# Kernel tuning notes

Hardware: AMD Instinct MI355X
Metric: run time of the kernel (lower is better)

## Reference

```python
import jax, jax.numpy as jnp
import numpy as np

SCALES = [1.0, 0.9, 1.1]


def conv2d(x, w, stride=1, pad=0):
    return jax.lax.conv_general_dilated(
        x, w, (stride, stride), [(pad, pad), (pad, pad)],
        dimension_numbers=('NCHW', 'OIHW', 'NCHW'))


def resize_hp(x, h, w):
    """Half-pixel bilinear == F.interpolate(mode='bilinear', align_corners=False)."""
    return jax.image.resize(x, x.shape[:-2] + (h, w), method='bilinear', antialias=False)


def upsample2x_ac(x):
    """align_corners=True bilinear 2x == nn.UpsamplingBilinear2d(scale_factor=2)."""
    def interp(arr, axis):
        n_in = arr.shape[axis]
        n_out = 2 * n_in
        pos = jnp.linspace(0.0, n_in - 1.0, n_out)
        i0 = jnp.floor(pos).astype(jnp.int32)
        i1 = jnp.minimum(i0 + 1, n_in - 1)
        t = (pos - i0.astype(pos.dtype)).astype(arr.dtype)
        shp = [1] * arr.ndim
        shp[axis] = n_out
        t = t.reshape(shp)
        return jnp.take(arr, i0, axis=axis) * (1 - t) + jnp.take(arr, i1, axis=axis) * t
    return interp(interp(x, 2), 3)


def backbone(images, fw1, fw2, fw3, fw4):
    # Stand-in for Resnet50FPN: two maps at stride 8 (512ch) and stride 16 (1024ch).
    x = jax.nn.relu(conv2d(images, fw1, 2, 3))   # stride 2
    x = jax.nn.relu(conv2d(x, fw2, 2, 1))        # stride 4
    f3 = jax.nn.relu(conv2d(x, fw3, 2, 1))       # stride 8,  C=512
    f4 = jax.nn.relu(conv2d(f3, fw4, 2, 1))      # stride 16, C=1024
    return [f3, f4]


def extract_features(image_features, tlbrs_np, H):
    # Faithful port of extract_features: per-batch/per-map/per-patch crop ->
    # bilinear resize -> multi-scale conv2d correlation. Crop coords come from
    # the concrete tlbrs array (data-dependent shapes, resolved at trace time).
    B, P, _ = tlbrs_np.shape
    batch_similarities = []
    for b in range(B):
        similarities = []
        for feat in image_features:
            fm = feat[b:b + 1]                                  # [1,FC,FH,FW]
            _, FC, FH, FW = fm.shape
            scaling = H / FH
            sc = tlbrs_np[b] / scaling
            tl = np.maximum(np.floor(sc[:, :2]), 0.0)
            br = np.ceil(sc[:, 2:]) + 1.0
            br[:, 0] = np.minimum(br[:, 0], FH)
            br[:, 1] = np.minimum(br[:, 1], FW)
            PH = int((br[:, 0] - tl[:, 0]).max())
            PW = int((br[:, 1] - tl[:, 1]).max())
            patches = []
            for p in range(P):
                top, left = int(tl[p, 0]), int(tl[p, 1])
                bot, right = int(br[p, 0]), int(br[p, 1])
                patches.append(resize_hp(fm[:, :, top:bot, left:right], PH, PW))
            patches = jnp.concatenate(patches, axis=0)          # [P,FC,PH,PW]
            for scale in SCALES:
                PHs = int(np.ceil(PH * scale))
                PWs = int(np.ceil(PW * scale))
                if PHs < 1:
                    PHs = PH
                if PWs < 1:
                    PWs = PW
                pf = resize_hp(patches, PHs, PWs)
                # F.pad(left=PWs//2, right=(PWs-1)//2, top=PHs//2, bottom=(PHs-1)//2)
                sim = jax.lax.conv_general_dilated(
                    fm, pf, (1, 1),
                    [(PHs // 2, (PHs - 1) // 2), (PWs // 2, (PWs - 1) // 2)],
                    dimension_numbers=('NCHW', 'OIHW', 'NCHW'))  # [1,P,FH,FW]
                sim = jnp.transpose(sim, (1, 0, 2, 3))           # [P,1,FH,FW]
                similarities.append(resize_hp(sim, FH, FW))
        SH = max(s_.shape[2] for s_ in similarities)
        SW = max(s_.shape[3] for s_ in similarities)
        sims = jnp.concatenate([resize_hp(s_, SH, SW) for s_ in similarities], axis=1)
        batch_similarities.append(sims)                          # [P,S,SH,SW]
    return jnp.stack(batch_similarities, axis=0)                 # [B,P,S,SH,SW]


def count_regressor(x, rw1, rb1, rw2, rb2, rw3, rb3, rw4, rb4, rw5, rb5):
    bc = lambda v: v[None, :, None, None]
    x = jax.nn.relu(conv2d(x, rw1, 1, 3) + bc(rb1))   # 6  -> 196, k7 p3
    x = upsample2x_ac(x)
    x = jax.nn.relu(conv2d(x, rw2, 1, 2) + bc(rb2))   # 196 -> 128, k5 p2
    x = upsample2x_ac(x)
    x = jax.nn.relu(conv2d(x, rw3, 1, 1) + bc(rb3))   # 128 -> 64, k3 p1
    x = upsample2x_ac(x)
    x = jax.nn.relu(conv2d(x, rw4, 1, 0) + bc(rb4))   # 64  -> 32, k1
    x = jax.nn.relu(conv2d(x, rw5, 1, 0) + bc(rb5))   # 32  -> 1,  k1
    return x


def setup_inputs() -> dict:
    key = jax.random.key(0)
    ks = jax.random.split(key, 10)
    B, P, H, W = 2, 3, 384, 384

    def w(k, shape):
        fan_in = shape[1] * shape[2] * shape[3]
        return (jax.random.normal(k, shape, jnp.float32)
                * np.float32(np.sqrt(2.0 / fan_in)))

    images = jax.random.normal(ks[0], (B, 3, H, W), jnp.float32)
    rng = np.random.RandomState(0)
    t = rng.uniform(20, 260, (B, P))
    l = rng.uniform(20, 260, (B, P))
    bh = rng.uniform(32, 96, (B, P))
    bw = rng.uniform(32, 96, (B, P))
    tlbrs = jnp.asarray(
        np.stack([t, l, np.minimum(t + bh, H), np.minimum(l + bw, W)], axis=-1),
        jnp.float32)
    return dict(
        images=images, tlbrs=tlbrs,
        fw1=w(ks[1], (64, 3, 7, 7)), fw2=w(ks[2], (256, 64, 3, 3)),
        fw3=w(ks[3], (512, 256, 3, 3)), fw4=w(ks[4], (1024, 512, 3, 3)),
        rw1=w(ks[5], (196, 6, 7, 7)), rb1=jnp.zeros((196,), jnp.float32),
        rw2=w(ks[6], (128, 196, 5, 5)), rb2=jnp.zeros((128,), jnp.float32),
        rw3=w(ks[7], (64, 128, 3, 3)), rb3=jnp.zeros((64,), jnp.float32),
        rw4=w(ks[8], (32, 64, 1, 1)), rb4=jnp.zeros((32,), jnp.float32),
        rw5=w(ks[9], (1, 32, 1, 1)), rb5=jnp.zeros((1,), jnp.float32))


def reference(images, tlbrs, fw1, fw2, fw3, fw4,
              rw1, rb1, rw2, rb2, rw3, rb3, rw4, rb4, rw5, rb5):
    H = images.shape[2]
    feats = backbone(images, fw1, fw2, fw3, fw4)
    sims = extract_features(feats, np.asarray(tlbrs), H)        # [B,P,S,SH,SW]
    B, P, S, SH, SW = sims.shape
    x = sims.reshape(B * P, S, SH, SW)
    out = count_regressor(x, rw1, rb1, rw2, rb2, rw3, rb3, rw4, rb4, rw5, rb5)
    oh, ow = out.shape[2], out.shape[3]
    # pool='max' over the P exemplar maps, per batch element
    return out.reshape(B, P, 1, oh, ow).max(axis=1)             # [B,1,8*SH,8*SW]
```

## Files before the change

### kernel.cpp

```cpp
#include <hip/hip_runtime.h>
#include <math.h>

typedef _Float16 h8 __attribute__((ext_vector_type(8)));
typedef float f4 __attribute__((ext_vector_type(4)));

static const size_t OFF_SIMSH = 256;
static const size_t OFF_WB    = 98560;
static const size_t ARENA     = 3553536;
static const size_t IMH  = 3553536;
static const size_t B1H  = 4833536;
static const size_t B2H  = 7602432;
static const size_t F3H  = 10813696;
static const size_t F4H  = 13467904;
static const size_t PRAW = 15827200;
static const size_t PSC  = 18186496;
static const size_t SIMRAW = 27144448;
static const size_t WSIM = 27196288;
static const size_t R1H = 3553536;
static const size_t U1H = 6011136;
static const size_t R2H = 13537536;
static const size_t U2H = 17076480;
static const size_t R3H = 33683712;

static const size_t WB1 = 0;
static const size_t WB2 = 28672;
static const size_t WB3 = 176128;
static const size_t WB4 = 1355776;
static const size_t WR1 = 6074368;
static const size_t WR2 = 6189056;
static const size_t WR3 = 6836224;

__global__ __launch_bounds__(64) void k_meta(const float* __restrict__ tlbrs,
                                             int* __restrict__ meta)
{
    if (threadIdx.x != 0 || blockIdx.x != 0) return;
    const double SC[3] = {1.0, 0.9, 1.1};
    for (int b = 0; b < 2; ++b)
        for (int lvl = 0; lvl < 2; ++lvl) {
            int FH = lvl ? 24 : 48;
            float scaling = lvl ? 16.f : 8.f;
            int base = (b * 2 + lvl) * 32;
            int PH = 0, PW = 0;
            for (int p = 0; p < 3; ++p) {
                const float* t4 = tlbrs + (b * 3 + p) * 4;
                float st = t4[0] / scaling, sl = t4[1] / scaling;
                float sb = t4[2] / scaling, sr = t4[3] / scaling;
                int top  = (int)fmaxf(floorf(st), 0.f);
                int left = (int)fmaxf(floorf(sl), 0.f);
                int bot  = (int)fminf(ceilf(sb) + 1.f, (float)FH);
                int rgt  = (int)fminf(ceilf(sr) + 1.f, (float)FH);
                meta[base + p * 4 + 0] = top;
                meta[base + p * 4 + 1] = left;
                meta[base + p * 4 + 2] = bot;
                meta[base + p * 4 + 3] = rgt;
                PH = max(PH, bot - top);
                PW = max(PW, rgt - left);
            }
            meta[base + 12] = PH;
            meta[base + 13] = PW;
            for (int s = 0; s < 3; ++s) {
                int PHs = (int)ceil((double)PH * SC[s]);
                int PWs = (int)ceil((double)PW * SC[s]);
                if (PHs < 1) PHs = PH;
                if (PWs < 1) PWs = PW;
                meta[base + 14 + s * 2] = PHs;
                meta[base + 15 + s * 2] = PWs;
            }
        }
}

__device__ __forceinline__ void halo_zero(h8* base, int Hp, int Wp, int halo,
                                          int Cg, int N)
{
    int inner = Hp - 2 * halo;
    int frame = Hp * Wp - inner * inner;
    long total = (long)N * frame * Cg;
    long idx = (long)blockIdx.x * 256 + threadIdx.x;
    if (idx >= total) return;
    int cg = (int)(idx % Cg);
    long r = idx / Cg;
    int f = (int)(r % frame);
    int n = (int)(r / frame);
    int topN = halo * Wp;
    int y, x;
    if (f < topN) { y = f / Wp; x = f % Wp; }
    else if (f < 2 * topN) { int f2 = f - topN; y = Hp - halo + f2 / Wp; x = f2 % Wp; }
    else {
        int f3 = f - 2 * topN;
        int row = f3 / (2 * halo), rr = f3 - row * (2 * halo);
        y = halo + row;
        x = rr < halo ? rr : Wp - 2 * halo + rr;
    }
    h8 z;
#pragma unroll
    for (int j = 0; j < 8; ++j) z[j] = (_Float16)0.f;
    base[((long)n * Hp * Wp + (long)y * Wp + x) * Cg + cg] = z;
}

__global__ __launch_bounds__(256) void k_halos1(float* wsf)
{
    switch (blockIdx.y) {
    case 0: halo_zero((h8*)(wsf + IMH), 400, 400, 8, 1, 2); break;
    case 1: halo_zero((h8*)(wsf + B1H), 208, 208, 8, 8, 2); break;
    case 2: halo_zero((h8*)(wsf + B2H), 112, 112, 8, 32, 2); break;
    case 3: halo_zero((h8*)(wsf + F3H), 72, 72, 12, 64, 2); break;
    default: halo_zero((h8*)(wsf + F4H), 48, 48, 12, 128, 2); break;
    }
}

__global__ __launch_bounds__(256) void k_halos2(float* wsf)
{
    switch (blockIdx.y) {
    case 0: halo_zero((h8*)(wsf + OFF_SIMSH), 64, 64, 8, 1, 6); break;
    case 1: halo_zero((h8*)(wsf + R1H), 64, 64, 8, 25, 6); break;
    case 2: halo_zero((h8*)(wsf + U1H), 112, 112, 8, 25, 6); break;
    default: halo_zero((h8*)(wsf + U2H), 208, 208, 8, 16, 6); break;
    }
}

__global__ __launch_bounds__(256) void k_im2hwc(const float* __restrict__ img,
    _Float16* __restrict__ o)
{
    int idx = blockIdx.x * 256 + threadIdx.x;
    if (idx >= 2359296) return;
    int c = idx & 7;
    int pix = (idx >> 3) % 147456;
    int b = (idx >> 3) / 147456;
    int y = pix / 384, x = pix - y * 384;
    float v = (c < 3) ? img[((size_t)b * 3 + c) * 147456 + pix] : 0.f;
    o[((size_t)b * 1280000 + ((size_t)(y + 8) * 400 + (x + 8)) * 8) + c] = (_Float16)v;
}

__global__ __launch_bounds__(256) void k_wprepH(const float* __restrict__ w,
    _Float16* __restrict__ wB, int Cin, int KKt, int Cinp, int Cout, int Coutp,
    int total)
{
    int idx = blockIdx.x * 256 + threadIdx.x;
    if (idx >= total) return;
    int j = idx & 7;
    int co = (idx >> 3) % Coutp;
    int kq = idx / (8 * Coutp);
    int k = kq * 8 + j;
    int tap = k / Cinp, cip = k - tap * Cinp;
    float v = 0.f;
    if (tap < KKt && cip < Cin && co < Cout)
        v = w[((size_t)co * Cin + cip) * KKt + tap];
    wB[idx] = (_Float16)v;
}

template<int KK, int KW, int S, int CINP, int MT>
__global__ __launch_bounds__(256, 3) void k_convH(
    const _Float16* __restrict__ inI, int Winp, long inStride,
    const _Float16* __restrict__ wB, const float* __restrict__ bias,
    _Float16* __restrict__ outI, int Wop, long outStride,
    int Cout, int Coutp, int Wout, int pad, int Kpad, int storeC,
    float dsc, float osc)
{
    const int tid = threadIdx.x;
    const int n_img = blockIdx.z;
    const int m0 = blockIdx.x * (MT * 64);
    const int co0 = blockIdx.y * 64;
    const _Float16* inb = inI + (size_t)n_img * inStride;

    const int wv = tid >> 6, lane = tid & 63;
    const int lq = lane >> 4, lr = lane & 15;

    const _Float16* pb[MT];
#pragma unroll
    for (int mt = 0; mt < MT; ++mt) {
        int m = m0 + (wv * MT + mt) * 16 + lr;
        int y = m / Wout, x = m - y * Wout;
        pb[mt] = inb + ((long)(y * S - pad) * Winp + (x * S - pad)) * CINP;
    }
    const _Float16* wbc = wB + (size_t)(co0 + lr) * 8;

    f4 acc[MT][4];
#pragma unroll
    for (int i = 0; i < MT; ++i)
#pragma unroll
        for (int j = 0; j < 4; ++j) { f4 z = {0.f, 0.f, 0.f, 0.f}; acc[i][j] = z; }

    const int Kbat = Kpad >> 6;

    auto load_step = [&](int kb, h8* afX, h8* bfX) {
        int k0 = kb * 32 + lq * 8;
        int tap = k0 / CINP;
        int ci0 = k0 - tap * CINP;
        int dy = tap / KW, dx = tap - dy * KW;
        size_t kq = (size_t)(kb * 4 + lq) * Coutp;
#pragma unroll
        for (int nt = 0; nt < 4; ++nt)
            bfX[nt] = *(const h8*)(wbc + (kq + nt * 16) * 8);
        int doff = (dy * Winp + dx) * CINP + ci0;
#pragma unroll
        for (int mt = 0; mt < MT; ++mt)
            afX[mt] = *(const h8*)(pb[mt] + doff);
    };
    auto mfma_step = [&](h8* afX, h8* bfX) {
#pragma unroll
        for (int mt = 0; mt < MT; ++mt)
#pragma unroll
            for (int nt = 0; nt < 4; ++nt)
                acc[mt][nt] = __builtin_amdgcn_mfma_f32_16x16x32_f16(
                    afX[mt], bfX[nt], acc[mt][nt], 0, 0, 0);
    };
    auto load_batch = [&](int bb, h8 afX[2][MT > 0 ? MT : 1], h8 bfX[2][4]) {
        load_step(2 * bb, afX[0], bfX[0]);
        load_step(2 * bb + 1, afX[1], bfX[1]);
    };
    auto mfma_batch = [&](h8 afX[2][MT > 0 ? MT : 1], h8 bfX[2][4]) {
        mfma_step(afX[0], bfX[0]);
        mfma_step(afX[1], bfX[1]);
    };

    h8 afA[2][MT > 0 ? MT : 1], bfA[2][4], afB[2][MT > 0 ? MT : 1], bfB[2][4];
    load_batch(0, afA, bfA);
    int bb = 0;
    for (; bb + 1 < Kbat; bb += 2) {
        load_batch(bb + 1, afB, bfB);
        mfma_batch(afA, bfA);
        if (bb + 2 < Kbat) load_batch(bb + 2, afA, bfA);
        mfma_batch(afB, bfB);
    }
    if (bb < Kbat) mfma_batch(afA, bfA);

    _Float16* ob = outI + (size_t)n_img * outStride;
#pragma unroll
    for (int nt = 0; nt < 4; ++nt) {
        int co = co0 + nt * 16 + lr;
        if (co >= storeC) continue;
        bool valid = co < Cout;
        float bv = (bias && valid) ? bias[co] : 0.f;
#pragma unroll
        for (int mt = 0; mt < MT; ++mt) {
#pragma unroll
            for (int reg = 0; reg < 4; ++reg) {
                int m = m0 + (wv * MT + mt) * 16 + lq * 4 + reg;
                int y = m / Wout, x = m - y * Wout;
                float v = valid
                    ? fmaxf(fmaf(acc[mt][nt][reg], dsc, bv), 0.f) * osc : 0.f;
                ob[((long)y * Wop + x) * storeC + co] = (_Float16)v;
            }
        }
    }
}

__global__ __launch_bounds__(256) void k_praw(const _Float16* __restrict__ f3hI,
    const _Float16* __restrict__ f4hI, const int* __restrict__ meta,
    float* __restrict__ praw)
{
    int z = blockIdx.z;
    int p = z % 3, m = z / 3, lvl = m % 2, b = m / 2;
    int c = blockIdx.y;
    int FC = lvl ? 1024 : 512;
    if (c >= FC) return;
    int FHp = lvl ? 48 : 72;
    int fsh = lvl ? 10 : 9;
    const int* mb = meta + m * 32;
    int PH = mb[12], PW = mb[13];
    int oy = threadIdx.x / 16, ox = threadIdx.x % 16;
    if (oy >= PH || ox >= PW) return;
    int top = mb[p * 4 + 0], left = mb[p * 4 + 1];
    int bot = mb[p * 4 + 2], rgt = mb[p * 4 + 3];
    int h = bot - top, w = rgt - left;
    const _Float16* fm = lvl ? (f4hI + (size_t)b * 2359296)
                             : (f3hI + (size_t)b * 2654208);
    float sy = ((oy + 0.5f) * h) / PH - 0.5f;
    sy = fminf(fmaxf(sy, 0.f), (float)(h - 1));
    int y0 = (int)floorf(sy); float ty = sy - y0; int y1 = min(y0 + 1, h - 1);
    float sx = ((ox + 0.5f) * w) / PW - 0.5f;
    sx = fminf(fmaxf(sx, 0.f), (float)(w - 1));
    int x0 = (int)floorf(sx); float tx = sx - x0; int x1 = min(x0 + 1, w - 1);
    float v00 = (float)fm[((size_t)((top + y0) * FHp + (left + x0)) << fsh) + c];
    float v01 = (float)fm[((size_t)((top + y0) * FHp + (left + x1)) << fsh) + c];
    float v10 = (float)fm[((size_t)((top + y1) * FHp + (left + x0)) << fsh) + c];
    float v11 = (float)fm[((size_t)((top + y1) * FHp + (left + x1)) << fsh) + c];
    float v = (1.f - ty) * ((1.f - tx) * v00 + tx * v01)
            +        ty  * ((1.f - tx) * v10 + tx * v11);
    size_t base = (size_t)(b * 1179648 + (lvl ? 393216 : 0)) + ((size_t)p * FC + c) * 256;
    praw[base + oy * 16 + ox] = v;
}

__global__ __launch_bounds__(256) void k_psc(const float* __restrict__ praw,
    const int* __restrict__ meta, float* __restrict__ psc)
{
    int z = blockIdx.z;
    int p = z % 3, s = (z / 3) % 3, lvl = (z / 9) % 2, b = z / 18;
    int c = blockIdx.y;
    int FC = lvl ? 1024 : 512;
    if (c >= FC) return;
    const int* mb = meta + (b * 2 + lvl) * 32;
    int PH = mb[12], PW = mb[13];
    int PHs = mb[14 + s * 2], PWs = mb[15 + s * 2];
    int idx = blockIdx.x * 256 + threadIdx.x;
    int ys = idx / 18, xs = idx % 18;
    if (ys >= PHs || xs >= PWs) return;
    const float* src = praw + (size_t)(b * 1179648 + (lvl ? 393216 : 0))
                            + ((size_t)p * FC + c) * 256;
    float sy = ((ys + 0.5f) * PH) / PHs - 0.5f;
    sy = fminf(fmaxf(sy, 0.f), (float)(PH - 1));
    int y0 = (int)floorf(sy); float ty = sy - y0; int y1 = min(y0 + 1, PH - 1);
    float sx = ((xs + 0.5f) * PW) / PWs - 0.5f;
    sx = fminf(fmaxf(sx, 0.f), (float)(PW - 1));
    int x0 = (int)floorf(sx); float tx = sx - x0; int x1 = min(x0 + 1, PW - 1);
    float v = (1.f - ty) * ((1.f - tx) * src[y0 * 16 + x0] + tx * src[y0 * 16 + x1])
            +        ty  * ((1.f - tx) * src[y1 * 16 + x0] + tx * src[y1 * 16 + x1]);
    size_t base = (size_t)b * 4478976 + (lvl ? (1492992 + (size_t)s * 995328)
                                             : ((size_t)s * 497664));
    psc[base + ((size_t)p * FC + c) * 324 + ys * 18 + xs] = v;
}

__global__ __launch_bounds__(256) void k_fill0(float* p, int n)
{
    int i = blockIdx.x * 256 + threadIdx.x;
    if (i < n) p[i] = 0.f;
}

__global__ __launch_bounds__(256) void k_wsim(const float* __restrict__ psc,
    const int* __restrict__ meta, _Float16* __restrict__ W)
{
    int z = blockIdx.z;
    int lvl = z & 1, b = z >> 1;
    int FC = lvl ? 1024 : 512;
    int total = FC * 324 * 16;
    int e = blockIdx.x * 256 + threadIdx.x;
    if (e >= total) return;
    _Float16* Wz = W + (size_t)b * 7962624 + (lvl ? 2654208 : 0);
    int j = e & 7, n = (e >> 3) & 15, kq = e >> 7;
    int k = kq * 8 + j;
    int ci = k & 15;
    int tapcb = k >> 4;
    int tap = tapcb % 324;
    int cb = tapcb / 324;
    int c = cb * 16 + ci;
    int rr = tap / 18, cc = tap - rr * 18;
    float v = 0.f;
    if (n < 9) {
        int s = n / 3, p = n % 3;
        const int* mb = meta + z * 32;
        int PHs = mb[14 + s * 2], PWs = mb[15 + s * 2];
        int ky = rr - (9 - (PHs >> 1));
        int kx = cc - (9 - (PWs >> 1));
        if ((unsigned)ky < (unsigned)PHs && (unsigned)kx < (unsigned)PWs) {
            size_t base = (size_t)b * 4478976 + (lvl ? (1492992 + (size_t)s * 995328)
                                                     : ((size_t)s * 497664));
            v = psc[base + ((size_t)p * FC + c) * 324 + ky * 18 + kx];
        }
    }
    Wz[e] = (_Float16)v;
}

template<int TW, int FH, int FHP, int FC, int SROWS, int SCOLSU, bool LVL>
__global__ __launch_bounds__(256) void k_simS(
    const _Float16* __restrict__ fI, long fStride,
    const _Float16* __restrict__ Wb, float* __restrict__ simraw)
{
    __shared__ __align__(16) _Float16 As[2 * SROWS * SCOLSU * 8];
    const int M = FH * FH;
    const int PIX = TW * 64;
    const int b = blockIdx.z;
    const int mg = blockIdx.x;
    const int cb = blockIdx.y;
    const _Float16* fm = fI + (size_t)b * fStride;
    const _Float16* Wz = Wb + (size_t)b * 7962624 + (LVL ? 2654208 : 0)
                       + (size_t)cb * 82944;
    const int tid = threadIdx.x;
    const int y0row = (mg * PIX) / FH;

    const int count = 2 * SROWS * SCOLSU;
    for (int idx = tid; idx < count; idx += 256) {
        int half = idx / (SROWS * SCOLSU);
        int rem = idx - half * (SROWS * SCOLSU);
        int row = rem / SCOLSU, col = rem - row * SCOLSU;
        const _Float16* src = fm + ((long)(y0row + row - 9) * FHP + (col - 9)) * FC
                            + cb * 16 + half * 8;
        *(h8*)&As[idx * 8] = *(const h8*)src;
    }
    __syncthreads();

    const int wv = tid >> 6, lane = tid & 63;
    const int lq = lane >> 4, lr = lane & 15;
    int abase[TW];
#pragma unroll
    for (int i = 0; i < TW; ++i) {
        int st = mg * (4 * TW) + wv + 4 * i;
        int m = st * 16 + lr;
        int py = m / FH - y0row, px = m - (m / FH) * FH;
        abase[i] = ((lq & 1) * SROWS + py) * SCOLSU + px;
    }
    const int thalf = lq >> 1;

    f4 acc[TW];
#pragma unroll
    for (int i = 0; i < TW; ++i) { f4 z = {0.f, 0.f, 0.f, 0.f}; acc[i] = z; }

    auto load_step = [&](int step, h8* avX, h8& bfX) {
        int tap = step * 2 + thalf;
        int dy = tap / 18, dx = tap - dy * 18;
        bfX = *(const h8*)(Wz + ((size_t)(step * 4 + lq) * 16 + lr) * 8);
        int doff = dy * SCOLSU + dx;
#pragma unroll
        for (int i = 0; i < TW; ++i)
            avX[i] = *(const h8*)&As[(size_t)(abase[i] + doff) * 8];
    };
    auto mfma_step = [&](h8* avX, h8 bfX) {
#pragma unroll
        for (int i = 0; i < TW; ++i)
            acc[i] = __builtin_amdgcn_mfma_f32_16x16x32_f16(avX[i], bfX, acc[i], 0, 0, 0);
    };

    h8 avA[TW], avB[TW], bfA, bfB;
    load_step(0, avA, bfA);
    int kb = 0;
    for (; kb + 1 < 162; kb += 2) {
        load_step(kb + 1, avB, bfB);
        mfma_step(avA, bfA);
        if (kb + 2 < 162) load_step(kb + 2, avA, bfA);
        mfma_step(avB, bfB);
    }
    if (kb < 162) mfma_step(avA, bfA);

    if (lr < 9) {
        int s = lr / 3, p = lr - s * 3;
        float* base = simraw + (size_t)b * 25920
                    + (LVL ? (20736 + (size_t)s * 1728) : ((size_t)s * 6912))
                    + (size_t)p * M;
#pragma unroll
        for (int i = 0; i < TW; ++i) {
            int st = mg * (4 * TW) + wv + 4 * i;
            int row0 = st * 16 + lq * 4;
#pragma unroll
            for (int r = 0; r < 4; ++r) {
                int m = row0 + r;
                if (m < M) atomicAdd(base + m, acc[i][r]);
            }
        }
    }
}

__global__ __launch_bounds__(256) void k_sims(const float* __restrict__ simraw,
    _Float16* __restrict__ simshI)
{
    int idx = blockIdx.x * 256 + threadIdx.x;
    if (idx >= 110592) return;
    int scat = idx & 7;
    int rest = idx >> 3;
    int x = rest % 48, y = (rest / 48) % 48;
    int p = (rest / 2304) % 3, b = rest / 6912;
    float v = 0.f;
    if (scat < 6) {
        int lvl = scat / 3, s = scat % 3;
        if (lvl == 0) {
            v = simraw[(size_t)b * 25920 + (size_t)s * 6912 + (size_t)p * 2304 + y * 48 + x];
        } else {
            const float* src = simraw + (size_t)b * 25920 + 20736 + (size_t)s * 1728
                                      + (size_t)p * 576;
            float sy = (y + 0.5f) * 0.5f - 0.5f; sy = fminf(fmaxf(sy, 0.f), 23.f);
            int y0 = (int)floorf(sy); float ty = sy - y0; int y1 = min(y0 + 1, 23);
            float sx = (x + 0.5f) * 0.5f - 0.5f; sx = fminf(fmaxf(sx, 0.f), 23.f);
            int x0 = (int)floorf(sx); float tx = sx - x0; int x1 = min(x0 + 1, 23);
            v = (1.f - ty) * ((1.f - tx) * src[y0 * 24 + x0] + tx * src[y0 * 24 + x1])
              +        ty  * ((1.f - tx) * src[y1 * 24 + x0] + tx * src[y1 * 24 + x1]);
        }
    }
    int n = b * 3 + p;
    simshI[((size_t)n * 32768 + ((size_t)y * 64 + x) * 8) + scat]
        = (_Float16)(v * 0.0009765625f);
}

__global__ __launch_bounds__(256) void k_up2acH(const h8* __restrict__ inI,
    int inWp, long inStride, h8* __restrict__ outI, int outWp, long outStride,
    int N_, int Hin, int Win, int Cg)
{
    int Hout = 2 * Hin, Wout = 2 * Win;
    size_t total = (size_t)N_ * Hout * Wout * Cg;
    size_t idx = (size_t)blockIdx.x * 256 + threadIdx.x;
    if (idx >= total) return;
    int cg = (int)(idx % Cg);
    size_t r = idx / Cg;
    int x = (int)(r % Wout);
    int y = (int)((r / Wout) % Hout);
    int n = (int)(r / ((size_t)Wout * Hout));
    int dh = 2 * Hin - 1, dw = 2 * Win - 1;
    int ay = y * (Hin - 1);
    int y0 = ay / dh; int y1 = min(y0 + 1, Hin - 1);
    float ty = (float)(ay - y0 * dh) / (float)dh;
    int ax = x * (Win - 1);
    int x0 = ax / dw; int x1 = min(x0 + 1, Win - 1);
    float tx = (float)(ax - x0 * dw) / (float)dw;
    const h8* base = inI + (size_t)n * inStride;
    h8 a = base[((size_t)y0 * inWp + x0) * Cg + cg];
    h8 b8 = base[((size_t)y0 * inWp + x1) * Cg + cg];
    h8 c8 = base[((size_t)y1 * inWp + x0) * Cg + cg];
    h8 d8 = base[((size_t)y1 * inWp + x1) * Cg + cg];
    float w00 = (1.f - ty) * (1.f - tx), w01 = (1.f - ty) * tx;
    float w10 = ty * (1.f - tx), w11 = ty * tx;
    h8 o;
#pragma unroll
    for (int j = 0; j < 8; ++j)
        o[j] = (_Float16)(w00 * (float)a[j] + w01 * (float)b8[j]
                        + w10 * (float)c8[j] + w11 * (float)d8[j]);
    outI[(size_t)n * outStride + ((size_t)y * outWp + x) * Cg + cg] = o;
}

__global__ __launch_bounds__(256) void k_final(const h8* __restrict__ r3h,
    const float* __restrict__ w4, const float* __restrict__ b4,
    const float* __restrict__ w5, const float* __restrict__ b5,
    float* __restrict__ out)
{
    __shared__ float sw4[2048];
    __shared__ float sb4[32];
    __shared__ float sw5[32];
    int tid = threadIdx.x;
    for (int i = tid; i < 2048; i += 256) sw4[i] = w4[i];
    if (tid < 32) { sb4[tid] = b4[tid]; sw5[tid] = w5[tid]; }
    __syncthreads();
    int idx = blockIdx.x * 256 + tid;
    int x = idx % 384, y = (idx / 384) % 384, b = idx / 147456;
    int ay = y * 191; int y0 = ay / 383; int y1 = min(y0 + 1, 191);
    float ty = (float)(ay - y0 * 383) / 383.f;
    int ax = x * 191; int x0 = ax / 383; int x1 = min(x0 + 1, 191);
    float tx = (float)(ax - x0 * 383) / 383.f;
    float w00 = (1.f - ty) * (1.f - tx), w01 = (1.f - ty) * tx;
    float w10 = ty * (1.f - tx), w11 = ty * tx;
    float best = 0.f;
    for (int p = 0; p < 3; ++p) {
        int n = b * 3 + p;
        float acc[32];
#pragma unroll
        for (int co = 0; co < 32; ++co) acc[co] = sb4[co];
        const h8* rb = r3h + (size_t)n * 36864 * 8;
        for (int cg = 0; cg < 8; ++cg) {
            h8 a00 = rb[(size_t)(y0 * 192 + x0) * 8 + cg];
            h8 a01 = rb[(size_t)(y0 * 192 + x1) * 8 + cg];
            h8 a10 = rb[(size_t)(y1 * 192 + x0) * 8 + cg];
            h8 a11 = rb[(size_t)(y1 * 192 + x1) * 8 + cg];
#pragma unroll
            for (int jj = 0; jj < 8; ++jj) {
                float v = (w00 * (float)a00[jj] + w01 * (float)a01[jj]
                         + w10 * (float)a10[jj] + w11 * (float)a11[jj]) * 64.f;
                int ci = cg * 8 + jj;
#pragma unroll
                for (int co = 0; co < 32; ++co)
                    acc[co] = fmaf(sw4[co * 64 + ci], v, acc[co]);
            }
        }
        float s5 = b5[0];
#pragma unroll
        for (int co = 0; co < 32; ++co)
            s5 = fmaf(fmaxf(acc[co], 0.f), sw5[co], s5);
        s5 = fmaxf(s5, 0.f);
        best = fmaxf(best, s5);
    }
    out[idx] = best;
}

extern "C" void kernel_launch(void* const* d_in, const int* in_sizes, int n_in,
                              void* d_out, int out_size, void* d_ws, size_t ws_size,
                              hipStream_t stream)
{
    (void)in_sizes; (void)n_in; (void)out_size; (void)ws_size;
    const float* images = (const float*)d_in[0];
    const float* tlbrs  = (const float*)d_in[1];
    const float* fw1 = (const float*)d_in[2];
    const float* fw2 = (const float*)d_in[3];
    const float* fw3 = (const float*)d_in[4];
    const float* fw4 = (const float*)d_in[5];
    const float* rw1 = (const float*)d_in[6];
    const float* rb1 = (const float*)d_in[7];
    const float* rw2 = (const float*)d_in[8];
    const float* rb2 = (const float*)d_in[9];
    const float* rw3 = (const float*)d_in[10];
    const float* rb3 = (const float*)d_in[11];
    const float* rw4 = (const float*)d_in[12];
    const float* rb4 = (const float*)d_in[13];
    const float* rw5 = (const float*)d_in[14];
    const float* rb5 = (const float*)d_in[15];
    float* wsf = (float*)d_ws;
    int* meta = (int*)d_ws;
    float* out = (float*)d_out;
    _Float16* wb = (_Float16*)(wsf + OFF_WB);

    _Float16* imhI   = (_Float16*)(wsf + IMH)  + (8 * 400 + 8) * 8;
    _Float16* b1hI   = (_Float16*)(wsf + B1H)  + (8 * 208 + 8) * 64;
    _Float16* b2hI   = (_Float16*)(wsf + B2H)  + (8 * 112 + 8) * 256;
    _Float16* f3hI   = (_Float16*)(wsf + F3H)  + (12 * 72 + 12) * 512;
    _Float16* f4hI   = (_Float16*)(wsf + F4H)  + (12 * 48 + 12) * 1024;
    _Float16* simshI = (_Float16*)(wsf + OFF_SIMSH) + (8 * 64 + 8) * 8;
    _Float16* r1hI   = (_Float16*)(wsf + R1H)  + (8 * 64 + 8) * 200;
    _Float16* u1hI   = (_Float16*)(wsf + U1H)  + (8 * 112 + 8) * 200;
    _Float16* r2h    = (_Float16*)(wsf + R2H);
    _Float16* u2hI   = (_Float16*)(wsf + U2H)  + (8 * 208 + 8) * 128;
    _Float16* r3h    = (_Float16*)(wsf + R3H);
    _Float16* wsim   = (_Float16*)(wsf + WSIM);

    const float INV64 = 1.f / 64.f;

    hipLaunchKernelGGL(k_halos1, dim3(1728, 5), dim3(256), 0, stream, wsf);
    hipLaunchKernelGGL(k_meta, dim3(1), dim3(64), 0, stream, tlbrs, meta);
    hipLaunchKernelGGL(k_im2hwc, dim3(9216), dim3(256), 0, stream, images,
        (_Float16*)(wsf + IMH));

    hipLaunchKernelGGL(k_wprepH, dim3(112), dim3(256), 0, stream,
        fw1, wb + WB1, 3, 49, 8, 64, 64, 28672);
    hipLaunchKernelGGL(k_wprepH, dim3(576), dim3(256), 0, stream,
        fw2, wb + WB2, 64, 9, 64, 256, 256, 147456);
    hipLaunchKernelGGL(k_wprepH, dim3(4608), dim3(256), 0, stream,
        fw3, wb + WB3, 256, 9, 256, 512, 512, 1179648);
    hipLaunchKernelGGL(k_wprepH, dim3(18432), dim3(256), 0, stream,
        fw4, wb + WB4, 512, 9, 512, 1024, 1024, 4718592);
    hipLaunchKernelGGL(k_wprepH, dim3(448), dim3(256), 0, stream,
        rw1, wb + WR1, 6, 49, 8, 196, 256, 114688);
    hipLaunchKernelGGL(k_wprepH, dim3(2528), dim3(256), 0, stream,
        rw2, wb + WR2, 196, 25, 200, 128, 128, 647168);
    hipLaunchKernelGGL(k_wprepH, dim3(288), dim3(256), 0, stream,
        rw3, wb + WR3, 128, 9, 128, 64, 64, 73728);

    hipLaunchKernelGGL((k_convH<49, 7, 2, 8, 2>), dim3(288, 1, 2), dim3(256), 0, stream,
        imhI, 400, 1280000L, wb + WB1, (const float*)nullptr,
        b1hI, 208, 2768896L, 64, 64, 192, 3, 448, 64, 1.f, 1.f);
    hipLaunchKernelGGL((k_convH<9, 3, 2, 64, 2>), dim3(72, 4, 2), dim3(256), 0, stream,
        b1hI, 208, 2768896L, wb + WB2, (const float*)nullptr,
        b2hI, 112, 3211264L, 256, 256, 96, 1, 576, 256, 1.f, 1.f);
    hipLaunchKernelGGL((k_convH<9, 3, 2, 256, 2>), dim3(18, 8, 2), dim3(256), 0, stream,
        b2hI, 112, 3211264L, wb + WB3, (const float*)nullptr,
        f3hI, 72, 2654208L, 512, 512, 48, 1, 2304, 512, 1.f, 1.f);
    hipLaunchKernelGGL((k_convH<9, 3, 2, 512, 1>), dim3(9, 16, 2), dim3(256), 0, stream,
        f3hI, 72, 2654208L, wb + WB4, (const float*)nullptr,
        f4hI, 48, 2359296L, 1024, 1024, 24, 1, 4608, 1024, 1.f, 1.f);

    hipLaunchKernelGGL(k_praw, dim3(1, 1024, 12), dim3(256), 0, stream,
        f3hI, f4hI, meta, wsf + PRAW);
    hipLaunchKernelGGL(k_psc, dim3(2, 1024, 36), dim3(256), 0, stream,
        wsf + PRAW, meta, wsf + PSC);
    hipLaunchKernelGGL(k_wsim, dim3(20736, 1, 4), dim3(256), 0, stream,
        wsf + PSC, meta, wsim);
    hipLaunchKernelGGL(k_fill0, dim3(203), dim3(256), 0, stream,
        wsf + SIMRAW, 51840);
    hipLaunchKernelGGL((k_simS<3, 48, 72, 512, 21, 65, false>),
        dim3(12, 32, 2), dim3(256), 0, stream,
        f3hI, 2654208L, wsim, wsf + SIMRAW);
    hipLaunchKernelGGL((k_simS<1, 24, 48, 1024, 21, 41, true>),
        dim3(9, 64, 2), dim3(256), 0, stream,
        f4hI, 2359296L, wsim, wsf + SIMRAW);
    hipLaunchKernelGGL(k_sims, dim3(432), dim3(256), 0, stream,
        wsf + SIMRAW, simshI);
    hipLaunchKernelGGL(k_halos2, dim3(2400, 4), dim3(256), 0, stream, wsf);

    hipLaunchKernelGGL((k_convH<49, 7, 1, 8, 2>), dim3(18, 4, 6), dim3(256), 0, stream,
        simshI, 64, 32768L, wb + WR1, rb1,
        r1hI, 64, 819200L, 196, 256, 48, 3, 448, 200, 1024.f, INV64);
    hipLaunchKernelGGL(k_up2acH, dim3(5400), dim3(256), 0, stream,
        (const h8*)r1hI, 64, 102400L, (h8*)u1hI, 112, 313600L, 6, 48, 48, 25);
    hipLaunchKernelGGL((k_convH<25, 5, 1, 200, 2>), dim3(72, 2, 6), dim3(256), 0, stream,
        u1hI, 112, 2508800L, wb + WR2, rb2,
        r2h, 96, 1179648L, 128, 128, 96, 2, 5056, 128, 64.f, INV64);
    hipLaunchKernelGGL(k_up2acH, dim3(13824), dim3(256), 0, stream,
        (const h8*)r2h, 96, 147456L, (h8*)u2hI, 208, 692224L, 6, 96, 96, 16);
    hipLaunchKernelGGL((k_convH<9, 3, 1, 128, 2>), dim3(288, 1, 6), dim3(256), 0, stream,
        u2hI, 208, 5537792L, wb + WR3, rb3,
        r3h, 192, 2359296L, 64, 64, 192, 1, 1152, 64, 64.f, INV64);
    hipLaunchKernelGGL(k_final, dim3(1152), dim3(256), 0, stream,
        (const h8*)r3h, rw4, rb4, rw5, rb5, out);
}
```

Before: 981.1 us.

## Add split-K partial sums to under-occupied convolutions with reduction kernel

The conv kernel now splits its K-loop across extra blocks along grid y and writes fp32 partial accumulators to workspace. A new reduction kernel sums the partials and applies bias, ReLU and scaling before storing fp16. The split is applied to the backbone convs 2-4 and to the second regressor conv, whose grids were small relative to the CU count. To free workspace for the partials, the U2H halo zeroing is moved later. The cost is extra fp32 global traffic and more kernel launches.

Measured after the change: 957.4 us. 1.02x faster.

```diff
diff --git a/kernel.cpp b/kernel.cpp
--- a/kernel.cpp
+++ b/kernel.cpp
@@ -2,6 +2,7 @@
 #include <math.h>
 
 typedef _Float16 h8 __attribute__((ext_vector_type(8)));
+typedef _Float16 h4 __attribute__((ext_vector_type(4)));
 typedef float f4 __attribute__((ext_vector_type(4)));
 
 static const size_t OFF_SIMSH = 256;
@@ -21,6 +22,8 @@
 static const size_t R2H = 13537536;
 static const size_t U2H = 17076480;
 static const size_t R3H = 33683712;
+static const size_t PCONV = PRAW;
+static const size_t PR2   = U2H;
 
 static const size_t WB1 = 0;
 static const size_t WB2 = 28672;
@@ -108,14 +111,18 @@
     }
 }
 
-__global__ __launch_bounds__(256) void k_halos2(float* wsf)
+__global__ __launch_bounds__(256) void k_halos2a(float* wsf)
 {
     switch (blockIdx.y) {
     case 0: halo_zero((h8*)(wsf + OFF_SIMSH), 64, 64, 8, 1, 6); break;
     case 1: halo_zero((h8*)(wsf + R1H), 64, 64, 8, 25, 6); break;
-    case 2: halo_zero((h8*)(wsf + U1H), 112, 112, 8, 25, 6); break;
-    default: halo_zero((h8*)(wsf + U2H), 208, 208, 8, 16, 6); break;
-    }
+    default: halo_zero((h8*)(wsf + U1H), 112, 112, 8, 25, 6); break;
+    }
+}
+
+__global__ __launch_bounds__(256) void k_halos2b(float* wsf)
+{
+    halo_zero((h8*)(wsf + U2H), 208, 208, 8, 16, 6);
 }
 
 __global__ __launch_bounds__(256) void k_im2hwc(const float* __restrict__ img,
@@ -154,12 +161,13 @@
     const _Float16* __restrict__ wB, const float* __restrict__ bias,
     _Float16* __restrict__ outI, int Wop, long outStride,
     int Cout, int Coutp, int Wout, int pad, int Kpad, int storeC,
-    float dsc, float osc)
+    float dsc, float osc, int coBlocks, int kbatPer, float* partial)
 {
     const int tid = threadIdx.x;
     const int n_img = blockIdx.z;
     const int m0 = blockIdx.x * (MT * 64);
-    const int co0 = blockIdx.y * 64;
+    const int ks  = blockIdx.y / coBlocks;
+    const int co0 = (blockIdx.y - ks * coBlocks) * 64;
     const _Float16* inb = inI + (size_t)n_img * inStride;
 
     const int wv = tid >> 6, lane = tid & 63;
@@ -181,6 +189,8 @@
         for (int j = 0; j < 4; ++j) { f4 z = {0.f, 0.f, 0.f, 0.f}; acc[i][j] = z; }
 
     const int Kbat = Kpad >> 6;
+    const int bb0 = ks * kbatPer;
+    const int bb1 = min(Kbat, bb0 + kbatPer);
 
     auto load_step = [&](int kb, h8* afX, h8* bfX) {
         int k0 = kb * 32 + lq * 8;
@@ -214,15 +224,35 @@
     };
 
     h8 afA[2][MT > 0 ? MT : 1], bfA[2][4], afB[2][MT > 0 ? MT : 1], bfB[2][4];
-    load_batch(0, afA, bfA);
-    int bb = 0;
-    for (; bb + 1 < Kbat; bb += 2) {
+    load_batch(bb0, afA, bfA);
+    int bb = bb0;
+    for (; bb + 1 < bb1; bb += 2) {
         load_batch(bb + 1, afB, bfB);
         mfma_batch(afA, bfA);
-        if (bb + 2 < Kbat) load_batch(bb + 2, afA, bfA);
+        if (bb + 2 < bb1) load_batch(bb + 2, afA, bfA);
         mfma_batch(afB, bfB);
     }
-    if (bb < Kbat) mfma_batch(afA, bfA);
+    if (bb < bb1) mfma_batch(afA, bfA);
+
+    if (partial) {
+        const int Mtot = gridDim.x * (MT * 64);
+        const int C = coBlocks * 64;
+        const size_t chunk = (size_t)gridDim.z * Mtot * C;
+        float* pp = partial + (size_t)ks * chunk + (size_t)n_img * Mtot * C;
+#pragma unroll
+        for (int nt = 0; nt < 4; ++nt) {
+            int co = co0 + nt * 16 + lr;
+#pragma unroll
+            for (int mt = 0; mt < MT; ++mt) {
+#pragma unroll
+                for (int reg = 0; reg < 4; ++reg) {
+                    int m = m0 + (wv * MT + mt) * 16 + lq * 4 + reg;
+                    pp[(size_t)m * C + co] = acc[mt][nt][reg];
+                }
+            }
+        }
+        return;
+    }
 
     _Float16* ob = outI + (size_t)n_img * outStride;
 #pragma unroll
@@ -243,6 +273,34 @@
             }
         }
     }
+}
+
+__global__ __launch_bounds__(256) void k_redH(const float* __restrict__ partial,
+    long chunk, int KS, const float* __restrict__ bias,
+    _Float16* __restrict__ outI, int Wop, long outStride, int Wout,
+    int C, int M, int N, float dsc, float osc)
+{
+    long idx4 = (long)blockIdx.x * 256 + threadIdx.x;
+    long total4 = (long)N * M * C / 4;
+    if (idx4 >= total4) return;
+    long e = idx4 * 4;
+    int co = (int)(e % C);
+    long r = e / C;
+    int m = (int)(r % M);
+    int n = (int)(r / M);
+    f4 s = *(const f4*)(partial + e);
+    for (int ks = 1; ks < KS; ++ks) {
+        f4 t = *(const f4*)(partial + (size_t)ks * chunk + e);
+        s += t;
+    }
+    h4 o;
+#pragma unroll
+    for (int j = 0; j < 4; ++j) {
+        float bv = bias ? bias[co + j] : 0.f;
+        o[j] = (_Float16)(fmaxf(fmaf(s[j], dsc, bv), 0.f) * osc);
+    }
+    int y = m / Wout, x = m - y * Wout;
+    *(h4*)&outI[(size_t)n * outStride + ((size_t)y * Wop + x) * C + co] = o;
 }
 
 __global__ __launch_bounds__(256) void k_praw(const _Float16* __restrict__ f3hI,
@@ -593,6 +651,8 @@
     _Float16* u2hI   = (_Float16*)(wsf + U2H)  + (8 * 208 + 8) * 128;
     _Float16* r3h    = (_Float16*)(wsf + R3H);
     _Float16* wsim   = (_Float16*)(wsf + WSIM);
+    float* pconv = wsf + PCONV;
+    float* pr2   = wsf + PR2;
 
     const float INV64 = 1.f / 64.f;
 
@@ -618,16 +678,29 @@
 
     hipLaunchKernelGGL((k_convH<49, 7, 2, 8, 2>), dim3(288, 1, 2), dim3(256), 0, stream,
         imhI, 400, 1280000L, wb + WB1, (const float*)nullptr,
-        b1hI, 208, 2768896L, 64, 64, 192, 3, 448, 64, 1.f, 1.f);
-    hipLaunchKernelGGL((k_convH<9, 3, 2, 64, 2>), dim3(72, 4, 2), dim3(256), 0, stream,
+        b1hI, 208, 2768896L, 64, 64, 192, 3, 448, 64, 1.f, 1.f,
+        1, 7, (float*)nullptr);
+    hipLaunchKernelGGL((k_convH<9, 3, 2, 64, 2>), dim3(72, 8, 2), dim3(256), 0, stream,
         b1hI, 208, 2768896L, wb + WB2, (const float*)nullptr,
-        b2hI, 112, 3211264L, 256, 256, 96, 1, 576, 256, 1.f, 1.f);
-    hipLaunchKernelGGL((k_convH<9, 3, 2, 256, 2>), dim3(18, 8, 2), dim3(256), 0, stream,
+        b2hI, 112, 3211264L, 256, 256, 96, 1, 576, 256, 1.f, 1.f,
+        4, 5, pconv);
+    hipLaunchKernelGGL(k_redH, dim3(4608), dim3(256), 0, stream,
+        pconv, 4718592L, 2, (const float*)nullptr,
+        b2hI, 112, 3211264L, 96, 256, 9216, 2, 1.f, 1.f);
+    hipLaunchKernelGGL((k_convH<9, 3, 2, 256, 2>), dim3(18, 32, 2), dim3(256), 0, stream,
         b2hI, 112, 3211264L, wb + WB3, (const float*)nullptr,
-        f3hI, 72, 2654208L, 512, 512, 48, 1, 2304, 512, 1.f, 1.f);
-    hipLaunchKernelGGL((k_convH<9, 3, 2, 512, 1>), dim3(9, 16, 2), dim3(256), 0, stream,
+        f3hI, 72, 2654208L, 512, 512, 48, 1, 2304, 512, 1.f, 1.f,
+        8, 9, pconv);
+    hipLaunchKernelGGL(k_redH, dim3(2304), dim3(256), 0, stream,
+        pconv, 2359296L, 4, (const float*)nullptr,
+        f3hI, 72, 2654208L, 48, 512, 2304, 2, 1.f, 1.f);
+    hipLaunchKernelGGL((k_convH<9, 3, 2, 512, 1>), dim3(9, 64, 2), dim3(256), 0, stream,
         f3hI, 72, 2654208L, wb + WB4, (const float*)nullptr,
-        f4hI, 48, 2359296L, 1024, 1024, 24, 1, 4608, 1024, 1.f, 1.f);
+        f4hI, 48, 2359296L, 1024, 1024, 24, 1, 4608, 1024, 1.f, 1.f,
+        16, 18, pconv);
+    hipLaunchKernelGGL(k_redH, dim3(1152), dim3(256), 0, stream,
+        pconv, 1179648L, 4, (const float*)nullptr,
+        f4hI, 48, 2359296L, 24, 1024, 576, 2, 1.f, 1.f);
 
     hipLaunchKernelGGL(k_praw, dim3(1, 1024, 12), dim3(256), 0, stream,
         f3hI, f4hI, meta, wsf + PRAW);
@@ -645,21 +718,28 @@
         f4hI, 2359296L, wsim, wsf + SIMRAW);
     hipLaunchKernelGGL(k_sims, dim3(432), dim3(256), 0, stream,
         wsf + SIMRAW, simshI);
-    hipLaunchKernelGGL(k_halos2, dim3(2400, 4), dim3(256), 0, stream, wsf);
+    hipLaunchKernelGGL(k_halos2a, dim3(2400, 3), dim3(256), 0, stream, wsf);
 
     hipLaunchKernelGGL((k_convH<49, 7, 1, 8, 2>), dim3(18, 4, 6), dim3(256), 0, stream,
         simshI, 64, 32768L, wb + WR1, rb1,
-        r1hI, 64, 819200L, 196, 256, 48, 3, 448, 200, 1024.f, INV64);
+        r1hI, 64, 819200L, 196, 256, 48, 3, 448, 200, 1024.f, INV64,
+        4, 7, (float*)nullptr);
     hipLaunchKernelGGL(k_up2acH, dim3(5400), dim3(256), 0, stream,
         (const h8*)r1hI, 64, 102400L, (h8*)u1hI, 112, 313600L, 6, 48, 48, 25);
-    hipLaunchKernelGGL((k_convH<25, 5, 1, 200, 2>), dim3(72, 2, 6), dim3(256), 0, stream,
+    hipLaunchKernelGGL((k_convH<25, 5, 1, 200, 2>), dim3(72, 4, 6), dim3(256), 0, stream,
         u1hI, 112, 2508800L, wb + WR2, rb2,
-        r2h, 96, 1179648L, 128, 128, 96, 2, 5056, 128, 64.f, INV64);
+        r2h, 96, 1179648L, 128, 128, 96, 2, 5056, 128, 64.f, INV64,
+        2, 40, pr2);
+    hipLaunchKernelGGL(k_redH, dim3(6912), dim3(256), 0, stream,
+        pr2, 7077888L, 2, rb2,
+        r2h, 96, 1179648L, 96, 128, 9216, 6, 64.f, INV64);
+    hipLaunchKernelGGL(k_halos2b, dim3(2400), dim3(256), 0, stream, wsf);
     hipLaunchKernelGGL(k_up2acH, dim3(13824), dim3(256), 0, stream,
         (const h8*)r2h, 96, 147456L, (h8*)u2hI, 208, 692224L, 6, 96, 96, 16);
     hipLaunchKernelGGL((k_convH<9, 3, 1, 128, 2>), dim3(288, 1, 6), dim3(256), 0, stream,
         u2hI, 208, 5537792L, wb + WR3, rb3,
-        r3h, 192, 2359296L, 64, 64, 192, 1, 1152, 64, 64.f, INV64);
+        r3h, 192, 2359296L, 64, 64, 192, 1, 1152, 64, 64.f, INV64,
+        1, 18, (float*)nullptr);
     hipLaunchKernelGGL(k_final, dim3(1152), dim3(256), 0, stream,
         (const h8*)r3h, rw4, rb4, rw5, rb5, out);
 }
```
